# Kernel optimization log

Measured on AMD Instinct MI355X. Metric: run time of the kernel, lower is better.

## Reference

```python
import jax, jax.numpy as jnp
import numpy as np

DIM = 768
HEADS = 12
HEAD_DIM = DIM // HEADS  # 64
THETA = 10000.0
B, S = 2, 2048


def rotate_half(x):
    # pairs-interleaved rotate: (x1, x2) -> (-x2, x1)
    xp = x.reshape(x.shape[:-1] + (-1, 2))
    x1, x2 = xp[..., 0], xp[..., 1]
    return jnp.stack((-x2, x1), axis=-1).reshape(x.shape)


def rope_freqs(seq_len, head_dim, dtype):
    inv = 1.0 / (THETA ** (jnp.arange(0, head_dim, 2, dtype=jnp.float32) / head_dim))
    pos = jnp.arange(seq_len, dtype=jnp.float32)
    f = pos[:, None] * inv[None, :]              # [S, head_dim//2]
    f = jnp.repeat(f, 2, axis=-1)                # [S, head_dim]
    return f.astype(dtype)


def apply_rotary(freqs, t):
    # freqs [S, D] broadcasts against t [B, H, S, D]
    return t * jnp.cos(freqs) + rotate_half(t) * jnp.sin(freqs)


def setup_inputs() -> dict:
    key = jax.random.key(0)
    k1, k2, k3 = jax.random.split(key, 3)
    x = jax.random.normal(k1, (B, S, DIM), dtype=jnp.float32)
    W_qkv = jax.random.normal(k2, (3 * DIM, DIM), dtype=jnp.float32) * 0.02
    W_proj = jax.random.normal(k3, (DIM, DIM), dtype=jnp.float32) * 0.02
    b_proj = jnp.zeros((DIM,), dtype=jnp.float32)
    return {"x": x, "W_qkv": W_qkv, "W_proj": W_proj, "b_proj": b_proj}


def reference(x, W_qkv, W_proj, b_proj):
    Bb, Ss, C = x.shape
    qkv = jnp.einsum('bsc,oc->bso', x, W_qkv)                    # [B,S,3C]
    qkv = qkv.reshape(Bb, Ss, 3, HEADS, HEAD_DIM)
    qkv = jnp.transpose(qkv, (2, 0, 3, 1, 4))                    # [3,B,H,S,D]
    q, k, v = qkv[0], qkv[1], qkv[2]
    freqs = rope_freqs(Ss, HEAD_DIM, x.dtype)
    q = apply_rotary(freqs, q)
    k = apply_rotary(freqs, k)
    scale = HEAD_DIM ** -0.5
    scores = jnp.einsum('bhqd,bhkd->bhqk', q, k) * scale         # [B,H,S,S]
    probs = jax.nn.softmax(scores, axis=-1)
    out = jnp.einsum('bhqk,bhkd->bhqd', probs, v)                # [B,H,S,D]
    out = jnp.transpose(out, (0, 2, 1, 3)).reshape(Bb, Ss, C)
    return jnp.einsum('bsc,oc->bso', out, W_proj) + b_proj
```

## Files before the change

kernel.cpp:

```cpp
#include <hip/hip_runtime.h>
#include <math.h>

#define Bq 2
#define Sq 2048
#define Cq 768
#define Hq 12
#define Dq 64

#define PANEL_SHORTS 98304
#define PANELS_X  32
#define PANELS_WQ 18
#define PANELS_WP 6

#define NROWS 49152
#define OPHALF 3145728
#define SPLIT_BLOCKS 2688
#define SM_SHIFT 8.0f

typedef _Float16 f16x8 __attribute__((ext_vector_type(8)));
typedef __fp16 fp16v2 __attribute__((ext_vector_type(2)));
typedef float f32x4 __attribute__((ext_vector_type(4)));
#define MFMA16F(a, b, c) __builtin_amdgcn_mfma_f32_16x16x32_f16(a, b, c, 0, 0, 0)

#define SCALEQ 0.18033688011112042f

static __device__ inline unsigned short f16bits(float x) {
    _Float16 h = (_Float16)x;
    return __builtin_bit_cast(unsigned short, h);
}
static __device__ inline unsigned int pk16(float a, float b) {
    fp16v2 h = __builtin_amdgcn_cvt_pkrtz(a, b);
    return __builtin_bit_cast(unsigned int, h);
}

static __device__ inline void gld_lds16(const unsigned short* g, unsigned short* l) {
    __builtin_amdgcn_global_load_lds(
        (const __attribute__((address_space(1))) unsigned int*)g,
        (__attribute__((address_space(3))) unsigned int*)l, 16, 0, 0);
}

__global__ __launch_bounds__(256) void split_kernel(
    const float* __restrict__ x, const float* __restrict__ wq,
    const float* __restrict__ wp,
    unsigned short* __restrict__ xs, unsigned short* __restrict__ wqs,
    unsigned short* __restrict__ wps,
    float* __restrict__ ctab, float* __restrict__ stab)
{
    if (blockIdx.x >= SPLIT_BLOCKS) {
        int idx = (blockIdx.x - SPLIT_BLOCKS) * 256 + threadIdx.x;
        int s = idx >> 5;
        int i = idx & 31;
        double f = (double)s * exp(-(double)i * 0.28782313662425573);
        ctab[idx] = (float)cos(f);
        stab[idx] = (float)sin(f);
        return;
    }
    const int cid  = blockIdx.x * 256 + threadIdx.x;
    const int panel = cid / 12288;
    const int pos8  = cid % 12288;
    const int step = pos8 >> 10;
    const int rem  = pos8 & 1023;
    const int J    = rem >> 6;
    const int lane = rem & 63;
    const int rowp = J * 8 + (lane >> 3);
    const int lc   = (lane & 7) ^ (rowp & 7);
    const int k    = step * 64 + lc * 8;
    const float* src; unsigned short* dst; int prow;
    if (panel < PANELS_X) {
        src = x;  dst = xs;  prow = panel;
    } else if (panel < PANELS_X + PANELS_WQ) {
        src = wq; dst = wqs; prow = panel - PANELS_X;
    } else {
        src = wp; dst = wps; prow = panel - PANELS_X - PANELS_WQ;
    }
    const int row = prow * 128 + rowp;
    float4 v0 = *(const float4*)(src + (size_t)row * Cq + k);
    float4 v1 = *(const float4*)(src + (size_t)row * Cq + k + 4);
    unsigned short o[8] = { f16bits(v0.x), f16bits(v0.y), f16bits(v0.z),
                            f16bits(v0.w), f16bits(v1.x), f16bits(v1.y),
                            f16bits(v1.z), f16bits(v1.w) };
    *(uint4*)&dst[(size_t)prow * PANEL_SHORTS + (size_t)pos8 * 8] = *(uint4*)o;
}

template <int MODE, int BM, int BN>
__global__ __launch_bounds__(256) void gemm_mfma_kernel(
    const unsigned short* __restrict__ Apr, const unsigned short* __restrict__ Bpr,
    const float* __restrict__ ctab, const float* __restrict__ stab,
    unsigned short* __restrict__ qp, unsigned short* __restrict__ kp,
    unsigned short* __restrict__ vp,
    float* __restrict__ out0, const float* __restrict__ bias)
{
    constexpr int MI  = BM / 32;
    constexpr int NI  = BN / 32;
    constexpr int WTM = BM / 2;
    constexpr int WTN = BN / 2;
    constexpr int BCH = BN / 8;
    constexpr int ACH = BM / 8;
    constexpr int CPW = (ACH + BCH) / 4;

    __shared__ unsigned short sA[BM * 64];
    __shared__ unsigned short sB[BN * 64];

    const int t    = threadIdx.x;
    const int w    = t >> 6;
    const int lane = t & 63;
    const int ml   = lane & 15;
    const int quad = lane >> 4;
    const int wm   = w >> 1;
    const int wn   = w & 1;

    const int mBase = blockIdx.y * BM;
    const int nBase = blockIdx.x * BN;

    const unsigned short* gpanA = Apr + (size_t)(mBase >> 7) * PANEL_SHORTS;
    const unsigned short* gpanB = Bpr + (size_t)(nBase >> 7) * PANEL_SHORTS;
    const int JbA = (mBase & 127) >> 3;
    const int JbB = (nBase & 127) >> 3;

    f32x4 acc[MI][NI];
    #pragma unroll
    for (int mi = 0; mi < MI; ++mi)
        #pragma unroll
        for (int ni = 0; ni < NI; ++ni)
            acc[mi][ni] = (f32x4){0.f, 0.f, 0.f, 0.f};

    for (int k0 = 0; k0 < 12; ++k0) {
        __syncthreads();
        #pragma unroll
        for (int cc = 0; cc < CPW; ++cc) {
            const int c = w * CPW + cc;
            if (c < BCH) {
                gld_lds16(gpanB + k0 * 8192 + (JbB + c) * 512 + lane * 8,
                          sB + c * 512);
            } else {
                const int a = c - BCH;
                gld_lds16(gpanA + k0 * 8192 + (JbA + a) * 512 + lane * 8,
                          sA + a * 512);
            }
        }
        __syncthreads();

        f16x8 aF[MI][2], bF[NI][2];
        #pragma unroll
        for (int mi = 0; mi < MI; ++mi) {
            const int row = wm * WTM + mi * 16 + ml;
            #pragma unroll
            for (int ks = 0; ks < 2; ++ks)
                aF[mi][ks] = *(const f16x8*)
                    &sA[row * 64 + (((ks * 4 + quad) ^ (row & 7)) << 3)];
        }
        #pragma unroll
        for (int ni = 0; ni < NI; ++ni) {
            const int row = wn * WTN + ni * 16 + ml;
            #pragma unroll
            for (int ks = 0; ks < 2; ++ks)
                bF[ni][ks] = *(const f16x8*)
                    &sB[row * 64 + (((ks * 4 + quad) ^ (row & 7)) << 3)];
        }
        #pragma unroll
        for (int mi = 0; mi < MI; ++mi)
            #pragma unroll
            for (int ni = 0; ni < NI; ++ni) {
                acc[mi][ni] = MFMA16F(aF[mi][0], bF[ni][0], acc[mi][ni]);
                acc[mi][ni] = MFMA16F(aF[mi][1], bF[ni][1], acc[mi][ni]);
            }
    }

    if (MODE == 0) {
        const int which = nBase / Cq;
        #pragma unroll
        for (int mi = 0; mi < MI; ++mi) {
            const int gm = mBase + wm * WTM + mi * 16 + quad * 4;
            const int bb = gm >> 11;
            const int s0 = gm & 2047;
            #pragma unroll
            for (int ni = 0; ni < NI; ++ni) {
                const int gn = nBase + wn * WTN + ni * 16 + ml;
                const int c  = gn - which * Cq;
                const int hh = c >> 6;
                const int dd = c & 63;
                const size_t hb = (size_t)(bb * Hq + hh);
                if (which < 2) {
                    #pragma unroll
                    for (int r = 0; r < 4; ++r) {
                        float val = acc[mi][ni][r];
                        float pv  = __shfl_xor(val, 1, 64);
                        const int fi = (s0 + r) * 32 + (dd >> 1);
                        float c0 = ctab[fi], sn = stab[fi];
                        float o = (dd & 1) ? (val * c0 + pv * sn)
                                           : (val * c0 - pv * sn);
                        if (which == 0) {
                            o *= SCALEQ;
                            qp[(hb * Sq + s0 + r) * 64 + dd] = f16bits(o);
                        } else {
                            const int ss = s0 + r, rr = ss & 63, kt2 = ss >> 6;
                            kp[(hb * 32 + kt2) * 4096 + rr * 64
                               + (((dd >> 3) ^ (rr & 7)) << 3) + (dd & 7)] = f16bits(o);
                        }
                    }
                } else {
                    unsigned short hv[4];
                    #pragma unroll
                    for (int r = 0; r < 4; ++r)
                        hv[r] = f16bits(acc[mi][ni][r]);
                    const int kt2 = s0 >> 6;
                    *(ushort4*)&vp[(hb * 32 + kt2) * 4096 + dd * 64
                        + ((((s0 & 63) >> 3) ^ (dd & 7)) << 3) + (s0 & 7)]
                        = *(ushort4*)hv;
                }
            }
        }
    } else {
        #pragma unroll
        for (int mi = 0; mi < MI; ++mi) {
            const int gm = mBase + wm * WTM + mi * 16 + quad * 4;
            #pragma unroll
            for (int ni = 0; ni < NI; ++ni) {
                const int gn = nBase + wn * WTN + ni * 16 + ml;
                const float bz = bias[gn];
                #pragma unroll
                for (int r = 0; r < 4; ++r)
                    out0[(size_t)(gm + r) * Cq + gn] = acc[mi][ni][r] + bz;
            }
        }
    }
}

__global__ __launch_bounds__(512, 6) void attn_mfma_kernel(
    const unsigned short* __restrict__ qp, const unsigned short* __restrict__ kp,
    const unsigned short* __restrict__ vp, unsigned short* __restrict__ op,
    float* __restrict__ lp)
{
    __shared__ __align__(16) unsigned short smem[24576];
    unsigned short* pb = smem + 16384;

    const int t    = threadIdx.x;
    const int w    = t >> 6;
    const int lane = t & 63;
    const int ml   = lane & 15;
    const int quad = lane >> 4;
    const int bi   = blockIdx.x;
    const int bh   = bi % 24;
    const int rest = bi / 24;
    const int qt   = rest >> 1;
    const int half = rest & 1;

    const bool isV = (w >= 4);
    const unsigned short* gsrc = isV ? vp : kp;
    const int Jb = (w & 3) * 2;
    const size_t gb = (size_t)bh * 131072;
    unsigned short* sMine = smem + (isV ? 8192 : 0);

    auto stage = [&](int buf, int kt) {
        const unsigned short* gt = gsrc + gb + (size_t)kt * 4096;
        unsigned short* sd = sMine + buf * 4096;
        #pragma unroll
        for (int j = 0; j < 2; ++j)
            gld_lds16(gt + (Jb + j) * 512 + lane * 8, sd + (Jb + j) * 512);
    };

    stage(0, half * 16);

    const size_t qrow = ((size_t)bh * Sq + qt * 128 + w * 16 + ml) * 64;
    f16x8 bQ[2];
    bQ[0] = *(const f16x8*)(qp + qrow + quad * 8);
    bQ[1] = *(const f16x8*)(qp + qrow + 32 + quad * 8);

    float l_st = 0.f;
    f32x4 O[4];
    #pragma unroll
    for (int ng = 0; ng < 4; ++ng) O[ng] = (f32x4){0.f, 0.f, 0.f, 0.f};

    unsigned short* pbl = pb + (w * 16 + ml) * 64;
    const int rsw = ml & 7;

    __syncthreads();

    for (int kt16 = 0; kt16 < 16; ++kt16) {
        const int cur = kt16 & 1;
        if (kt16 + 1 < 16) stage(cur ^ 1, half * 16 + kt16 + 1);
        const unsigned short* k_s = smem + cur * 4096;
        const unsigned short* v_s = smem + 8192 + cur * 4096;

        f32x4 S[4];
        #pragma unroll
        for (int ng = 0; ng < 4; ++ng) {
            const int row = ng * 16 + ml;
            f32x4 acc = (f32x4){-SM_SHIFT, -SM_SHIFT, -SM_SHIFT, -SM_SHIFT};
            #pragma unroll
            for (int ks = 0; ks < 2; ++ks) {
                f16x8 aK = *(const f16x8*)
                    &k_s[row * 64 + (((ks * 4 + quad) ^ (row & 7)) << 3)];
                acc = MFMA16F(aK, bQ[ks], acc);
            }
            S[ng] = acc;
        }

        #pragma unroll
        for (int ng = 0; ng < 4; ++ng) {
            float p0 = exp2f(S[ng][0]);
            float p1 = exp2f(S[ng][1]);
            float p2 = exp2f(S[ng][2]);
            float p3 = exp2f(S[ng][3]);
            l_st += (p0 + p1) + (p2 + p3);
            uint2 u;
            u.x = pk16(p0, p1);
            u.y = pk16(p2, p3);
            const int ch = ng * 2 + (quad >> 1);
            *(uint2*)&pbl[((ch ^ rsw) << 3) + (quad & 1) * 4] = u;
        }

        #pragma unroll
        for (int ks = 0; ks < 2; ++ks) {
            uint4 pu = *(const uint4*)&pbl[(((ks * 4 + quad) ^ rsw) << 3)];
            f16x8 bP = __builtin_bit_cast(f16x8, pu);
            #pragma unroll
            for (int ngd = 0; ngd < 4; ++ngd) {
                const int row = ngd * 16 + ml;
                f16x8 aV = *(const f16x8*)
                    &v_s[row * 64 + (((ks * 4 + quad) ^ (row & 7)) << 3)];
                O[ngd] = MFMA16F(aV, bP, O[ngd]);
            }
        }
        __syncthreads();
    }

    l_st += __shfl_xor(l_st, 16, 64);
    l_st += __shfl_xor(l_st, 32, 64);

    const int srow = qt * 128 + w * 16 + ml;
    const size_t rowb = (size_t)half * NROWS + (size_t)bh * 2048 + srow;
    if (quad == 0) lp[rowb] = l_st;
    const float il = 1.0f / l_st;
    #pragma unroll
    for (int ngd = 0; ngd < 4; ++ngd) {
        unsigned short o4[4];
        #pragma unroll
        for (int r = 0; r < 4; ++r)
            o4[r] = f16bits(O[ngd][r] * il);
        *(ushort4*)&op[rowb * 64 + ngd * 16 + quad * 4] = *(ushort4*)o4;
    }
}

__global__ __launch_bounds__(256) void combine_kernel(
    const unsigned short* __restrict__ op, const float* __restrict__ lp,
    unsigned short* __restrict__ attns)
{
    const int g   = blockIdx.x * 256 + threadIdx.x;
    const int row = g >> 3;
    const int ch  = g & 7;
    const int bh  = row >> 11;
    const int s   = row & 2047;

    const float l1v = lp[row];
    const float l2v = lp[NROWS + row];
    const float inv = 1.0f / (l1v + l2v);
    const float c1 = l1v * inv, c2 = l2v * inv;

    f16x8 h1 = *(const f16x8*)(op + (size_t)row * 64 + ch * 8);
    f16x8 h2 = *(const f16x8*)(op + OPHALF + (size_t)row * 64 + ch * 8);
    unsigned short o[8];
    #pragma unroll
    for (int j = 0; j < 8; ++j)
        o[j] = f16bits(c1 * (float)h1[j] + c2 * (float)h2[j]);

    const int bb = bh / Hq, hh = bh % Hq;
    const int mrow = bb * 2048 + s;
    const int panel = mrow >> 7, r128 = mrow & 127;
    const size_t addr = (size_t)panel * PANEL_SHORTS
                      + (r128 >> 3) * 512 + (r128 & 7) * 64
                      + (size_t)hh * 8192
                      + ((ch ^ (r128 & 7)) << 3);
    *(uint4*)&attns[addr] = *(uint4*)o;
}

extern "C" void kernel_launch(void* const* d_in, const int* in_sizes, int n_in,
                              void* d_out, int out_size, void* d_ws, size_t ws_size,
                              hipStream_t stream) {
    const float* x     = (const float*)d_in[0];
    const float* Wqkv  = (const float*)d_in[1];
    const float* Wproj = (const float*)d_in[2];
    const float* bproj = (const float*)d_in[3];
    float* out = (float*)d_out;

    char* p = (char*)d_ws;
    unsigned short* xs    = (unsigned short*)p; p += (size_t)PANELS_X  * PANEL_SHORTS * 2;
    unsigned short* wqs   = (unsigned short*)p; p += (size_t)PANELS_WQ * PANEL_SHORTS * 2;
    unsigned short* wps   = (unsigned short*)p; p += (size_t)PANELS_WP * PANEL_SHORTS * 2;
    unsigned short* qp    = (unsigned short*)p; p += (size_t)24 * Sq * 64 * 2;
    unsigned short* kp    = (unsigned short*)p; p += (size_t)24 * 131072 * 2;
    unsigned short* vp    = (unsigned short*)p; p += (size_t)24 * 131072 * 2;
    unsigned short* attns = (unsigned short*)p; p += (size_t)PANELS_X * PANEL_SHORTS * 2;
    unsigned short* op    = (unsigned short*)p; p += (size_t)2 * OPHALF * 2;
    float* lp             = (float*)p;          p += (size_t)2 * NROWS * 4;
    float* ctab = (float*)p; p += (size_t)Sq * 32 * 4;
    float* stab = (float*)p; p += (size_t)Sq * 32 * 4;

    split_kernel<<<SPLIT_BLOCKS + 256, 256, 0, stream>>>(
        x, Wqkv, Wproj, xs, wqs, wps, ctab, stab);
    gemm_mfma_kernel<0, 64, 128><<<dim3(18, 64), 256, 0, stream>>>(
        xs, wqs, ctab, stab, qp, kp, vp, nullptr, nullptr);
    attn_mfma_kernel<<<dim3(24 * 32), 512, 0, stream>>>(qp, kp, vp, op, lp);
    combine_kernel<<<dim3(1536), 256, 0, stream>>>(op, lp, attns);
    gemm_mfma_kernel<1, 64, 64><<<dim3(12, 64), 256, 0, stream>>>(
        attns, wps, ctab, stab, nullptr, nullptr, nullptr, out, bproj);
}
```

Before: 173.3 us.

## Process two query tiles per wave and split keys into four chunks

Each attention block now handles 256 query rows, with each wave owning two 16-row Q subtiles, so every K/V fragment loaded from shared memory feeds two MFMAs. Keys are split into quarters instead of halves to keep the grid size at 768 blocks, and the combine kernel merges four partial outputs weighted by their partial sums. The aim is to halve LDS traffic per MFMA and to raise MFMA density. In exchange it uses more registers (occupancy hint lowered from 6 to 4), more LDS for the P buffer, and twice the partial-output traffic written and read by the combine step.

Measured after the change: 176.0 us. No clear change (+1.6%).

```diff
diff --git a/kernel.cpp b/kernel.cpp
--- a/kernel.cpp
+++ b/kernel.cpp
@@ -13,7 +13,7 @@
 #define PANELS_WP 6
 
 #define NROWS 49152
-#define OPHALF 3145728
+#define OPQTR 3145728
 #define SPLIT_BLOCKS 2688
 #define SM_SHIFT 8.0f
 
@@ -226,12 +226,12 @@
     }
 }
 
-__global__ __launch_bounds__(512, 6) void attn_mfma_kernel(
+__global__ __launch_bounds__(512, 4) void attn_mfma_kernel(
     const unsigned short* __restrict__ qp, const unsigned short* __restrict__ kp,
     const unsigned short* __restrict__ vp, unsigned short* __restrict__ op,
     float* __restrict__ lp)
 {
-    __shared__ __align__(16) unsigned short smem[24576];
+    __shared__ __align__(16) unsigned short smem[32768];
     unsigned short* pb = smem + 16384;
 
     const int t    = threadIdx.x;
@@ -242,8 +242,8 @@
     const int bi   = blockIdx.x;
     const int bh   = bi % 24;
     const int rest = bi / 24;
-    const int qt   = rest >> 1;
-    const int half = rest & 1;
+    const int qt   = rest >> 2;
+    const int qtr  = rest & 3;
 
     const bool isV = (w >= 4);
     const unsigned short* gsrc = isV ? vp : kp;
@@ -259,86 +259,117 @@
             gld_lds16(gt + (Jb + j) * 512 + lane * 8, sd + (Jb + j) * 512);
     };
 
-    stage(0, half * 16);
-
-    const size_t qrow = ((size_t)bh * Sq + qt * 128 + w * 16 + ml) * 64;
-    f16x8 bQ[2];
-    bQ[0] = *(const f16x8*)(qp + qrow + quad * 8);
-    bQ[1] = *(const f16x8*)(qp + qrow + 32 + quad * 8);
-
-    float l_st = 0.f;
-    f32x4 O[4];
+    stage(0, qtr * 8);
+
+    const size_t qrow0 =
+        ((size_t)bh * Sq + qt * 256 + w * 32 + ml) * 64;
+    f16x8 bQ00 = *(const f16x8*)(qp + qrow0 + quad * 8);
+    f16x8 bQ01 = *(const f16x8*)(qp + qrow0 + 32 + quad * 8);
+    f16x8 bQ10 = *(const f16x8*)(qp + qrow0 + 16 * 64 + quad * 8);
+    f16x8 bQ11 = *(const f16x8*)(qp + qrow0 + 16 * 64 + 32 + quad * 8);
+
+    float l0 = 0.f, l1 = 0.f;
+    f32x4 O0[4], O1[4];
     #pragma unroll
-    for (int ng = 0; ng < 4; ++ng) O[ng] = (f32x4){0.f, 0.f, 0.f, 0.f};
-
-    unsigned short* pbl = pb + (w * 16 + ml) * 64;
+    for (int ng = 0; ng < 4; ++ng) {
+        O0[ng] = (f32x4){0.f, 0.f, 0.f, 0.f};
+        O1[ng] = (f32x4){0.f, 0.f, 0.f, 0.f};
+    }
+
+    unsigned short* pbl0 = pb + (w * 32 + ml) * 64;
+    unsigned short* pbl1 = pbl0 + 16 * 64;
     const int rsw = ml & 7;
 
     __syncthreads();
 
-    for (int kt16 = 0; kt16 < 16; ++kt16) {
-        const int cur = kt16 & 1;
-        if (kt16 + 1 < 16) stage(cur ^ 1, half * 16 + kt16 + 1);
+    for (int kt8 = 0; kt8 < 8; ++kt8) {
+        const int cur = kt8 & 1;
+        if (kt8 + 1 < 8) stage(cur ^ 1, qtr * 8 + kt8 + 1);
         const unsigned short* k_s = smem + cur * 4096;
         const unsigned short* v_s = smem + 8192 + cur * 4096;
 
-        f32x4 S[4];
+        f32x4 S0[4], S1[4];
         #pragma unroll
         for (int ng = 0; ng < 4; ++ng) {
             const int row = ng * 16 + ml;
-            f32x4 acc = (f32x4){-SM_SHIFT, -SM_SHIFT, -SM_SHIFT, -SM_SHIFT};
-            #pragma unroll
-            for (int ks = 0; ks < 2; ++ks) {
+            f32x4 a0 = (f32x4){-SM_SHIFT, -SM_SHIFT, -SM_SHIFT, -SM_SHIFT};
+            f32x4 a1 = (f32x4){-SM_SHIFT, -SM_SHIFT, -SM_SHIFT, -SM_SHIFT};
+            {
                 f16x8 aK = *(const f16x8*)
-                    &k_s[row * 64 + (((ks * 4 + quad) ^ (row & 7)) << 3)];
-                acc = MFMA16F(aK, bQ[ks], acc);
-            }
-            S[ng] = acc;
+                    &k_s[row * 64 + ((quad ^ (row & 7)) << 3)];
+                a0 = MFMA16F(aK, bQ00, a0);
+                a1 = MFMA16F(aK, bQ10, a1);
+            }
+            {
+                f16x8 aK = *(const f16x8*)
+                    &k_s[row * 64 + (((4 + quad) ^ (row & 7)) << 3)];
+                a0 = MFMA16F(aK, bQ01, a0);
+                a1 = MFMA16F(aK, bQ11, a1);
+            }
+            S0[ng] = a0; S1[ng] = a1;
         }
 
         #pragma unroll
         for (int ng = 0; ng < 4; ++ng) {
-            float p0 = exp2f(S[ng][0]);
-            float p1 = exp2f(S[ng][1]);
-            float p2 = exp2f(S[ng][2]);
-            float p3 = exp2f(S[ng][3]);
-            l_st += (p0 + p1) + (p2 + p3);
-            uint2 u;
-            u.x = pk16(p0, p1);
-            u.y = pk16(p2, p3);
-            const int ch = ng * 2 + (quad >> 1);
-            *(uint2*)&pbl[((ch ^ rsw) << 3) + (quad & 1) * 4] = u;
+            const int off = (((ng * 2 + (quad >> 1)) ^ rsw) << 3)
+                          + (quad & 1) * 4;
+            float p00 = exp2f(S0[ng][0]);
+            float p01 = exp2f(S0[ng][1]);
+            float p02 = exp2f(S0[ng][2]);
+            float p03 = exp2f(S0[ng][3]);
+            l0 += (p00 + p01) + (p02 + p03);
+            uint2 u0; u0.x = pk16(p00, p01); u0.y = pk16(p02, p03);
+            *(uint2*)&pbl0[off] = u0;
+            float p10 = exp2f(S1[ng][0]);
+            float p11 = exp2f(S1[ng][1]);
+            float p12 = exp2f(S1[ng][2]);
+            float p13 = exp2f(S1[ng][3]);
+            l1 += (p10 + p11) + (p12 + p13);
+            uint2 u1; u1.x = pk16(p10, p11); u1.y = pk16(p12, p13);
+            *(uint2*)&pbl1[off] = u1;
         }
 
         #pragma unroll
         for (int ks = 0; ks < 2; ++ks) {
-            uint4 pu = *(const uint4*)&pbl[(((ks * 4 + quad) ^ rsw) << 3)];
-            f16x8 bP = __builtin_bit_cast(f16x8, pu);
+            const int poff = ((ks * 4 + quad) ^ rsw) << 3;
+            uint4 pu0 = *(const uint4*)&pbl0[poff];
+            uint4 pu1 = *(const uint4*)&pbl1[poff];
+            f16x8 bP0 = __builtin_bit_cast(f16x8, pu0);
+            f16x8 bP1 = __builtin_bit_cast(f16x8, pu1);
             #pragma unroll
             for (int ngd = 0; ngd < 4; ++ngd) {
                 const int row = ngd * 16 + ml;
                 f16x8 aV = *(const f16x8*)
                     &v_s[row * 64 + (((ks * 4 + quad) ^ (row & 7)) << 3)];
-                O[ngd] = MFMA16F(aV, bP, O[ngd]);
+                O0[ngd] = MFMA16F(aV, bP0, O0[ngd]);
+                O1[ngd] = MFMA16F(aV, bP1, O1[ngd]);
             }
         }
         __syncthreads();
     }
 
-    l_st += __shfl_xor(l_st, 16, 64);
-    l_st += __shfl_xor(l_st, 32, 64);
-
-    const int srow = qt * 128 + w * 16 + ml;
-    const size_t rowb = (size_t)half * NROWS + (size_t)bh * 2048 + srow;
-    if (quad == 0) lp[rowb] = l_st;
-    const float il = 1.0f / l_st;
+    l0 += __shfl_xor(l0, 16, 64);
+    l1 += __shfl_xor(l1, 16, 64);
+    l0 += __shfl_xor(l0, 32, 64);
+    l1 += __shfl_xor(l1, 32, 64);
+
+    const int srow0 = qt * 256 + w * 32 + ml;
+    const size_t rb0 = (size_t)qtr * NROWS + (size_t)bh * 2048 + srow0;
+    const size_t rb1 = rb0 + 16;
+    if (quad == 0) { lp[rb0] = l0; lp[rb1] = l1; }
+    const float il0 = 1.0f / l0;
+    const float il1 = 1.0f / l1;
     #pragma unroll
     for (int ngd = 0; ngd < 4; ++ngd) {
         unsigned short o4[4];
         #pragma unroll
         for (int r = 0; r < 4; ++r)
-            o4[r] = f16bits(O[ngd][r] * il);
-        *(ushort4*)&op[rowb * 64 + ngd * 16 + quad * 4] = *(ushort4*)o4;
+            o4[r] = f16bits(O0[ngd][r] * il0);
+        *(ushort4*)&op[rb0 * 64 + ngd * 16 + quad * 4] = *(ushort4*)o4;
+        #pragma unroll
+        for (int r = 0; r < 4; ++r)
+            o4[r] = f16bits(O1[ngd][r] * il1);
+        *(ushort4*)&op[rb1 * 64 + ngd * 16 + quad * 4] = *(ushort4*)o4;
     }
 }
 
@@ -352,17 +383,23 @@
     const int bh  = row >> 11;
     const int s   = row & 2047;
 
-    const float l1v = lp[row];
-    const float l2v = lp[NROWS + row];
-    const float inv = 1.0f / (l1v + l2v);
-    const float c1 = l1v * inv, c2 = l2v * inv;
-
-    f16x8 h1 = *(const f16x8*)(op + (size_t)row * 64 + ch * 8);
-    f16x8 h2 = *(const f16x8*)(op + OPHALF + (size_t)row * 64 + ch * 8);
+    const float w0 = lp[row];
+    const float w1 = lp[NROWS + row];
+    const float w2 = lp[2 * NROWS + row];
+    const float w3 = lp[3 * NROWS + row];
+    const float inv = 1.0f / (((w0 + w1) + (w2 + w3)));
+
+    f16x8 h0 = *(const f16x8*)(op + (size_t)row * 64 + ch * 8);
+    f16x8 h1 = *(const f16x8*)(op + (size_t)OPQTR + (size_t)row * 64 + ch * 8);
+    f16x8 h2 = *(const f16x8*)(op + (size_t)2 * OPQTR + (size_t)row * 64 + ch * 8);
+    f16x8 h3 = *(const f16x8*)(op + (size_t)3 * OPQTR + (size_t)row * 64 + ch * 8);
     unsigned short o[8];
     #pragma unroll
-    for (int j = 0; j < 8; ++j)
-        o[j] = f16bits(c1 * (float)h1[j] + c2 * (float)h2[j]);
+    for (int j = 0; j < 8; ++j) {
+        float v = (w0 * (float)h0[j] + w1 * (float)h1[j])
+                + (w2 * (float)h2[j] + w3 * (float)h3[j]);
+        o[j] = f16bits(v * inv);
+    }
 
     const int bb = bh / Hq, hh = bh % Hq;
     const int mrow = bb * 2048 + s;
@@ -391,8 +428,8 @@
     unsigned short* kp    = (unsigned short*)p; p += (size_t)24 * 131072 * 2;
     unsigned short* vp    = (unsigned short*)p; p += (size_t)24 * 131072 * 2;
     unsigned short* attns = (unsigned short*)p; p += (size_t)PANELS_X * PANEL_SHORTS * 2;
-    unsigned short* op    = (unsigned short*)p; p += (size_t)2 * OPHALF * 2;
-    float* lp             = (float*)p;          p += (size_t)2 * NROWS * 4;
+    unsigned short* op    = (unsigned short*)p; p += (size_t)4 * OPQTR * 2;
+    float* lp             = (float*)p;          p += (size_t)4 * NROWS * 4;
     float* ctab = (float*)p; p += (size_t)Sq * 32 * 4;
     float* stab = (float*)p; p += (size_t)Sq * 32 * 4;
 
```
